# Optimization experiments

Hardware: AMD Instinct MI355X
Metric: run time of the kernel (lower is better)

Reference implementation:

```python
import jax, jax.numpy as jnp
import numpy as np
from jax import lax

B, N, C, CN, M, H, W = 2, 8192, 64, 64, 16, 180, 240
LN_EPS = 1e-5  # torch nn.LayerNorm([C]) default eps


def setup_inputs():
    key = jax.random.key(0)
    ks = jax.random.split(key, 20)
    x = jax.random.uniform(ks[0], (B, N)) * (W - 1)
    y = jax.random.uniform(ks[1], (B, N)) * (H - 1)
    t = jax.random.uniform(ks[2], (B, N))
    p = jnp.where(jax.random.uniform(ks[3], (B, N)) < 0.5, -1.0, 1.0)
    events = jnp.stack([x, y, t, p], axis=-1)  # [B,N,4]
    s = 0.05
    w = lambda k, shape: jax.random.normal(k, shape) * s
    return {
        "events": events,
        "W_mlp1": w(ks[4], (4, C)),
        "W_pe": w(ks[5], (4, CN)),
        "ln_w": jnp.ones((C,)),
        "ln_b": jnp.zeros((C,)),
        "lx_Wq": w(ks[6], (C, CN)), "lx_Wk": w(ks[7], (C, CN)),
        "lx_Wv": w(ks[8], (C, CN)), "lx_Wsa1": w(ks[9], (CN, 1)),
        "lx_Wsa2": w(ks[10], (CN, C)),
        "gx_Wq": w(ks[11], (C, CN)), "gx_Wk": w(ks[12], (C, CN)),
        "gx_Wv": w(ks[13], (C, CN)), "gx_Wpe": w(ks[14], (C, CN)),
        "gx_Wsa1": w(ks[15], (CN, 1)), "gx_Wsa2": w(ks[16], (CN, C)),
    }


def select_nearest(vect, m):
    # torch: F.pad(left=m//2, right=m//2-1) then unfold(dim=1, size=m, step=1)
    b, n, c = vect.shape
    pad = m // 2
    vp = jnp.pad(vect, ((0, 0), (pad, pad - 1), (0, 0)))
    idx = jnp.arange(n)[:, None] + jnp.arange(m)[None, :]  # [N,M]
    return vp[:, idx, :]  # [B,N,M,C]


def fps(event, npoint):
    # faithful farthest_point_sample_batch; masked_select returns the sampled
    # points in ORIGINAL index order, hence the sort of selected indices.
    b, n, c = event.shape
    bary = jnp.mean(event, axis=1, keepdims=True)
    farthest0 = jnp.argmax(jnp.sum((event - bary) ** 2, -1), axis=1)  # [B]
    dist0 = jnp.full((b, n), 1e10, event.dtype)

    def step(carry, _):
        distance, farthest = carry
        centroid = jnp.take_along_axis(event, farthest[:, None, None], axis=1)
        d = jnp.sum((event - centroid) ** 2, -1)
        distance = jnp.minimum(distance, d)  # distance[dist<distance]=dist
        return (distance, jnp.argmax(distance, axis=1)), farthest

    _, sel = lax.scan(step, (dist0, farthest0), None, length=npoint)
    sel = jnp.sort(sel.T, axis=1)  # [B,npoint], sorted index order
    return jnp.take_along_axis(event, sel[:, :, None], axis=1)  # [B,npoint,C]


def sub_attention(q, k_multi, v_multi, pe, Wsa1, Wsa2):
    # sa = q - k + pe -> Linear(Cn,1) -> softmax over M.
    # The original then computes matmul(scores[B,1,N,M], (v+pe)^T[B,Cn,M,N])
    # and sums over the last axis, which is exactly
    #   scores @ (sum_n (v_multi + pe))  -- computed here without the
    # [B,Cn,N,N] intermediate.
    sa = q[:, :, None, :] - k_multi + pe          # [B,N,M,Cn]
    logits = jnp.squeeze(sa @ Wsa1, -1)           # [B,N,M]
    scores = jax.nn.softmax(logits, axis=-1)
    S = jnp.sum(v_multi + pe, axis=1)             # [B,M,Cn]
    p_attn = jnp.einsum("bnm,bmc->bnc", scores, S)
    return p_attn @ Wsa2                          # [B,N,C]


def layer_norm(x, w, b):
    mu = jnp.mean(x, axis=-1, keepdims=True)
    var = jnp.var(x, axis=-1, keepdims=True)
    return (x - mu) / jnp.sqrt(var + LN_EPS) * w + b


def normalize_nonzero(space):
    # mean/std over nonzero entries (std unbiased, ddof=1 as torch.std)
    mask = space != 0
    cnt = jnp.sum(mask)
    mean = jnp.sum(jnp.where(mask, space, 0.0)) / jnp.maximum(cnt, 1)
    var = jnp.sum(jnp.where(mask, (space - mean) ** 2, 0.0)) / jnp.maximum(cnt - 1, 1)
    std = jnp.sqrt(var)
    centered = jnp.where(mask, space - mean, space)
    safe_std = jnp.where(std > 0, std, 1.0)
    normed = jnp.where(std > 0, centered / safe_std, centered)
    return jnp.where(cnt > 0, normed, space)


def events_to_image(feat, ev, ln_w, ln_b):
    # feat [N,C], ev [N,4]
    h = jax.nn.gelu(layer_norm(feat, ln_w, ln_b), approximate=False)
    xi = jnp.floor(ev[:, 0]).astype(jnp.int32)
    yi = jnp.floor(ev[:, 1]).astype(jnp.int32)
    p = ev[:, 3]
    flat = yi * W + xi
    space = jnp.zeros((H * W, h.shape[1]), h.dtype).at[flat].add(p[:, None] * h)
    return normalize_nonzero(space.reshape(H, W, -1))


def reference(events, W_mlp1, W_pe, ln_w, ln_b,
              lx_Wq, lx_Wk, lx_Wv, lx_Wsa1, lx_Wsa2,
              gx_Wq, gx_Wk, gx_Wv, gx_Wpe, gx_Wsa1, gx_Wsa2):
    b, n, _ = events.shape
    lx_in = events @ W_mlp1                                    # [B,N,C]
    # EventTransformer position encoding: unfold-neighbor differences in raw
    # 4-d event space, then Linear(4,Cn)
    pe = (events[:, :, None, :] - select_nearest(events, M)) @ W_pe  # [B,N,M,Cn]
    # LXformer
    q = lx_in @ lx_Wq
    k = lx_in @ lx_Wk
    v = lx_in @ lx_Wv
    lx_sa = sub_attention(q, select_nearest(k, M), select_nearest(v, M),
                          pe, lx_Wsa1, lx_Wsa2)
    lx_out = lx_in + lx_sa
    # GXformer: FPS-sampled global keys/values, FPS-based position encoding
    pe_g = (lx_out[:, :, None, :] - fps(lx_out, M)[:, None, :, :]) @ gx_Wpe
    qg = lx_out @ gx_Wq
    kg = lx_out @ gx_Wk
    vg = lx_out @ gx_Wv
    k_m = jnp.broadcast_to(fps(kg, M)[:, None], (b, n, M, CN))
    v_m = jnp.broadcast_to(fps(vg, M)[:, None], (b, n, M, CN))
    gx_sa = sub_attention(qg, k_m, v_m, pe_g, gx_Wsa1, gx_Wsa2)
    gx_out = lx_out + gx_sa
    # scatter events to image per batch element
    imgs = jax.vmap(lambda f, e: events_to_image(f, e, ln_w, ln_b))(gx_out, events)
    return jnp.transpose(imgs, (0, 3, 1, 2))  # [B,C,H,W]
```

## Files before the change

kernel.cpp:

```cpp
#include <hip/hip_runtime.h>


typedef unsigned short u16;
typedef unsigned long long ull;

#define NB 8192
#define IMG_H 180
#define IMG_W 240
#define HWPIX (IMG_H*IMG_W)
#define SPB (HWPIX*64)
#define NC (NB*64)

#define TT_AC    0
#define TT_T     16384
#define TT_W1    32768
#define TT_EDGEV 32960
#define TT_EDGEF 35008
#define TT_S     37056
#define TT_SEL   39104
#define TT_CG    45248
#define TT_ESUM  45376
#define TT_STATS 45408
#define TT_SYNC  45440
#define TT_GCNT  45632
#define TT_LXS   45664
#define TT_ZOFF  45376
#define TT_ZCNT  288
#define TT_TOT   45792

__device__ __forceinline__ float bf2f(u16 u){
  union { unsigned int i; float f; } w; w.i = ((unsigned int)u) << 16; return w.f;
}
__device__ __forceinline__ u16 f2bf(float f){
  union { unsigned int i; float f; } w; w.f = f;
  unsigned int x = w.i;
  x += 0x7fffu + ((x >> 16) & 1u);
  return (u16)(x >> 16);
}
__device__ __forceinline__ bool isbf(const void* ev){
  unsigned w3 = ((const unsigned*)ev)[3];
  return !(w3 == 0x3F800000u || w3 == 0xBF800000u);
}
__device__ __forceinline__ float ld(const void* p, int i, bool bf){
  return bf ? bf2f(((const u16*)p)[i]) : ((const float*)p)[i];
}
__device__ __forceinline__ void stout(void* o, long i, float v, bool bf){
  if (bf) ((u16*)o)[i] = f2bf(v); else ((float*)o)[i] = v;
}
__device__ __forceinline__ float waveSum(float v){
#pragma unroll
  for (int m = 1; m < 64; m <<= 1) v += __shfl_xor(v, m, 64);
  return v;
}
__device__ __forceinline__ ull waveMaxU64(ull v){
#pragma unroll
  for (int m = 1; m < 64; m <<= 1){
    ull o = (ull)__shfl_xor((long long)v, m, 64);
    if (o > v) v = o;
  }
  return v;
}
__device__ __forceinline__ ull packPDI(int phase, float d, int n){
  return ((ull)phase << 45) | ((ull)__float_as_uint(d) << 13) | (ull)(8191 - n);
}
__device__ __forceinline__ int unpackI(ull p){ return 8191 - (int)(p & 0x1FFFull); }

__global__ void kW(const void* __restrict__ ev, const void* __restrict__ Wq,
                   const void* __restrict__ Wk, const void* __restrict__ Wpe,
                   const void* __restrict__ w1, float* __restrict__ ws, int tail){
  const bool bf = isbf(ev);
  const int tid = threadIdx.x;
  for (int i = tid; i < TT_ZCNT; i += 256) ws[tail + TT_ZOFF + i] = 0.f;
  if (tid < 64){
    float s1 = 0.f, s2 = 0.f;
    for (int c = 0; c < 64; c++){
      float wc = ld(w1, c, bf);
      s1 += ld(Wq, tid*64 + c, bf) * wc;
      s2 += ld(Wk, tid*64 + c, bf) * wc;
    }
    ws[tail + TT_W1 + tid] = s1;
    ws[tail + TT_W1 + 64 + tid] = s2;
    if (tid < 4){
      float s3 = 0.f;
      for (int c = 0; c < 64; c++) s3 += ld(Wpe, tid*64 + c, bf) * ld(w1, c, bf);
      ws[tail + TT_W1 + 128 + tid] = s3;
    }
  }
}

__global__ void __launch_bounds__(256) kE(const void* __restrict__ ev,
    float* __restrict__ ws, int tail, int bb0){
  const bool bf = isbf(ev);
  const int bb = bb0 + blockIdx.z;
  const int lane = threadIdx.x & 63, w = threadIdx.x >> 6;
  float s0 = 0.f, s1 = 0.f, s2 = 0.f, s3 = 0.f;
#pragma unroll
  for (int j = 0; j < 4; j++){
    int r = blockIdx.x*256 + threadIdx.x + 2048*j;
    const int e4 = (bb*NB + r)*4;
    s0 += ld(ev, e4+0, bf); s1 += ld(ev, e4+1, bf);
    s2 += ld(ev, e4+2, bf); s3 += ld(ev, e4+3, bf);
  }
  s0 = waveSum(s0); s1 = waveSum(s1); s2 = waveSum(s2); s3 = waveSum(s3);
  __shared__ float r4[4][4];
  if (lane == 0){ r4[w][0]=s0; r4[w][1]=s1; r4[w][2]=s2; r4[w][3]=s3; }
  __syncthreads();
  if (threadIdx.x < 4)
    atomicAdd(&ws[tail + TT_ESUM + bb*16 + threadIdx.x],
              r4[0][threadIdx.x]+r4[1][threadIdx.x]+r4[2][threadIdx.x]+r4[3][threadIdx.x]);
}

__global__ void __launch_bounds__(256, 4) kA(const void* __restrict__ ev,
    const void* __restrict__ Wm, const void* __restrict__ Wpe,
    const void* __restrict__ Wv, float* __restrict__ ws,
    int offA, int strA, int tail, int bb0){
  const bool bf = isbf(ev);
  const int bb = bb0 + blockIdx.z;
  const int lane = threadIdx.x & 63, w = threadIdx.x >> 6;
  float* A = ws + offA + (size_t)bb*strA;
  const float wq1 = ws[tail + TT_W1 + lane];
  const float wk1 = ws[tail + TT_W1 + 64 + lane];
  const float wp10 = ws[tail+TT_W1+128], wp11 = ws[tail+TT_W1+129],
              wp12 = ws[tail+TT_W1+130], wp13 = ws[tail+TT_W1+131];
  const float wm0 = ld(Wm, 0*64+lane, bf), wm1 = ld(Wm, 1*64+lane, bf),
              wm2 = ld(Wm, 2*64+lane, bf), wm3 = ld(Wm, 3*64+lane, bf);
  const bool edgeBlk = (blockIdx.x == 0 || blockIdx.x == 1023);
#pragma unroll
  for (int i = 0; i < 2; i++){
    const int n = blockIdx.x*8 + w + 4*i;
    const int e4 = (bb*NB + n)*4;
    float e0 = ld(ev, e4+0, bf), e1 = ld(ev, e4+1, bf),
          e2 = ld(ev, e4+2, bf), e3 = ld(ev, e4+3, bf);
    float lx = e0*wm0 + e1*wm1 + e2*wm2 + e3*wm3;
    float epe = e0*wp10 + e1*wp11 + e2*wp12 + e3*wp13;
    float acv = waveSum(lx * wq1) + epe;
    float tv  = waveSum(lx * wk1) + epe;
    A[n*64 + lane] = lx;
    if (lane == 0){
      ws[tail + TT_AC + bb*8192 + n] = acv;
      ws[tail + TT_T  + bb*8192 + n] = tv;
    }
    if (edgeBlk && (n < 8 || n >= NB-8)){
      int e = (n < 8) ? n : (n - (NB-16));
      float v = 0.f;
      for (int cn = 0; cn < 64; cn++)
        v += __shfl(lx, cn, 64) * ld(Wv, cn*64 + lane, bf);
      float f = e0*ld(Wpe, lane, bf) + e1*ld(Wpe, 64+lane, bf)
              + e2*ld(Wpe, 128+lane, bf) + e3*ld(Wpe, 192+lane, bf);
      ws[tail + TT_EDGEV + bb*1024 + e*64 + lane] = v;
      ws[tail + TT_EDGEF + bb*1024 + e*64 + lane] = f;
    }
  }
}

__global__ void __launch_bounds__(64) kB(const void* __restrict__ ev,
    const void* __restrict__ Wm, const void* __restrict__ Wv,
    const void* __restrict__ Wsa2, float* __restrict__ ws, int tail, int bb0){
  const bool bf = isbf(ev);
  const int bb = bb0 + blockIdx.z;
  const int m = blockIdx.x, lane = threadIdx.x;
  float tm = 0.f;
#pragma unroll
  for (int i = 0; i < 4; i++) tm += ws[tail + TT_ESUM + bb*16 + i] * ld(Wm, i*64 + lane, bf);
  float vs0 = 0.f, vs1 = 0.f;
#pragma unroll
  for (int j = 0; j < 64; j += 2){
    vs0 += __shfl(tm, j, 64)   * ld(Wv, j*64 + lane, bf);
    vs1 += __shfl(tm, j+1, 64) * ld(Wv, (j+1)*64 + lane, bf);
  }
  float vsum = vs0 + vs1;
  const int d = m - 8;
  float sv = 0.f, sf = 0.f;
  const float* EV = ws + tail + TT_EDGEV + bb*1024;
  const float* EF = ws + tail + TT_EDGEF + bb*1024;
  if (d < 0){
    for (int e = 16 + d; e < 16; e++){ sv += EV[e*64+lane]; sf += EF[e*64+lane]; }
  } else {
    for (int e = 0; e < d; e++){ sv += EV[e*64+lane]; sf += EF[e*64+lane]; }
  }
  float S = vsum - sv + sf;
  float sw0 = 0.f, sw1 = 0.f;
#pragma unroll
  for (int c = 0; c < 64; c += 2){
    sw0 += __shfl(S, c, 64)   * ld(Wsa2, c*64 + lane, bf);
    sw1 += __shfl(S, c+1, 64) * ld(Wsa2, (c+1)*64 + lane, bf);
  }
  ws[tail + TT_S + bb*1024 + m*64 + lane] = sw0 + sw1;
}

__global__ void __launch_bounds__(256) kC(const void* __restrict__ ev,
    const void* __restrict__ gWk, const void* __restrict__ gWv,
    float* __restrict__ ws,
    int offA, int strA, int offB, int strB, int offC, int strC,
    int offLXP, int strLXP, int tail, int bb0){
  const bool bf = isbf(ev);
  const int bb = bb0 + blockIdx.z;
  float* A = ws + offA + (size_t)bb*strA;
  float* Bp = ws + offB + (size_t)bb*strB;
  float* Cp = ws + offC + (size_t)bb*strC;
  __shared__ float SW_lds[1024];
  __shared__ float WK[4096];
  __shared__ float WV[4096];
  __shared__ float lred[4][64];
  const int tid = threadIdx.x, lane = tid & 63, w = tid >> 6;
  for (int i = tid; i < 1024; i += 256) SW_lds[i] = ws[tail + TT_S + bb*1024 + i];
  for (int i = tid; i < 4096; i += 256){
    WK[i] = ld(gWk, i, bf);
    WV[i] = ld(gWv, i, bf);
  }
  __syncthreads();
  float lxoR[2];
  float lxsum = 0.f;
#pragma unroll
  for (int i = 0; i < 2; i++){
    const int n = blockIdx.x*8 + w + 4*i;
    float lx  = A[n*64 + lane];
    float acn = ws[tail + TT_AC + bb*8192 + n];
    const int m = lane & 15;
    const int j = n + m - 8;
    float tv = (j >= 0 && j < NB) ? ws[tail + TT_T + bb*8192 + j] : 0.f;
    float logit = acn - tv;
    float mx = logit;
#pragma unroll
    for (int k = 1; k < 16; k <<= 1) mx = fmaxf(mx, __shfl_xor(mx, k, 64));
    float ex = expf(logit - mx);
    float sm = ex;
#pragma unroll
    for (int k = 1; k < 16; k <<= 1) sm += __shfl_xor(sm, k, 64);
    float sig = ex / sm;
    float sa = 0.f;
#pragma unroll
    for (int mm = 0; mm < 16; mm++) sa += __shfl(sig, mm, 64) * SW_lds[mm*64 + lane];
    float lxo = lx + sa;
    lxoR[i] = lxo;
    Bp[n*64 + lane] = lxo;
    lxsum += lxo;
  }
  lred[w][lane] = lxsum;
#pragma unroll
  for (int i = 0; i < 2; i++){
    const int n = blockIdx.x*8 + w + 4*i;
    float k0 = 0.f, k1 = 0.f, v0 = 0.f, v1 = 0.f;
#pragma unroll
    for (int cn = 0; cn < 64; cn += 2){
      float x0 = __shfl(lxoR[i], cn, 64);
      float x1 = __shfl(lxoR[i], cn+1, 64);
      k0 += x0 * WK[cn*64 + lane];
      k1 += x1 * WK[(cn+1)*64 + lane];
      v0 += x0 * WV[cn*64 + lane];
      v1 += x1 * WV[(cn+1)*64 + lane];
    }
    A[n*64 + lane] = k0 + k1;
    Cp[n*64 + lane] = v0 + v1;
  }
  __syncthreads();
  if (tid < 64)
    ws[offLXP + (size_t)bb*strLXP + blockIdx.x*64 + tid] =
      lred[0][tid]+lred[1][tid]+lred[2][tid]+lred[3][tid];
}

__global__ void __launch_bounds__(512) kL(float* __restrict__ ws,
    int offLXP, int strLXP, int tail, int bb0){
  const int bb = bb0 + blockIdx.z;
  __shared__ float red[8][64];
  const int tid = threadIdx.x, c = tid & 63, grp = tid >> 6;
  const float* LXP = ws + offLXP + (size_t)bb*strLXP;
  float s = 0.f;
  for (int b2 = grp; b2 < 1024; b2 += 8) s += LXP[b2*64 + c];
  red[grp][c] = s;
  __syncthreads();
  if (tid < 64){
    float t = 0.f;
#pragma unroll
    for (int q = 0; q < 8; q++) t += red[q][tid];
    ws[tail + TT_LXS + bb*64 + tid] = t;
  }
}

__global__ void __launch_bounds__(512) kFPS(const void* __restrict__ ev,
    const void* __restrict__ gWk, const void* __restrict__ gWv,
    const void* __restrict__ gWpe, const void* __restrict__ gWsa1,
    const void* __restrict__ gWsa2, float* __restrict__ ws,
    int offA, int strA, int offB, int strB, int offC, int strC,
    int tail, int bb0){
  const int g = blockIdx.y, idx = blockIdx.x;
  const int bb = bb0 + blockIdx.z;
  const int tid = threadIdx.x, lane = tid & 63, w = tid >> 6;
  const float* pts = ws + (g == 0 ? offB + (size_t)bb*strB
                         : g == 1 ? offA + (size_t)bb*strA
                                  : offC + (size_t)bb*strC);
  ull* slot = (ull*)(ws + tail + TT_SYNC + (bb*3 + g)*32);
  int* gcnt = (int*)(ws + tail + TT_GCNT + bb*16);

  __shared__ float cent[64];
  __shared__ float lxsS[64];
  __shared__ ull   wvS[8];
  __shared__ int   selS[16];
  __shared__ int   sCur;
  __shared__ float gfS[1024];
  __shared__ float betaS[16];
  __shared__ float GS[64];

  const int n0 = idx*1024 + tid;
  float4 P[2][16];
#pragma unroll
  for (int j = 0; j < 2; j++)
#pragma unroll
    for (int i = 0; i < 16; i++)
      P[j][i] = ((const float4*)(pts + (size_t)(n0 + j*512)*64))[i];

  const bool bf = isbf(ev);
  if (tid < 64){
    float lxs = ws[tail + TT_LXS + bb*64 + tid];
    lxsS[tid] = lxs;
    float c;
    if (g == 0) c = lxs * (1.0f/NB);
    else {
      const void* W = (g == 1) ? gWk : gWv;
      float s = 0.f;
#pragma unroll
      for (int j = 0; j < 64; j++) s += __shfl(lxs, j, 64) * ld(W, j*64 + tid, bf);
      c = s * (1.0f/NB);
    }
    cent[tid] = c;
  }
  __syncthreads();

  const float4* cv = (const float4*)cent;
  float md[2] = {1e10f, 1e10f};
  int cur;

  {
    float dd[2];
#pragma unroll
    for (int j = 0; j < 2; j++){
      float d = 0.f;
#pragma unroll
      for (int i = 0; i < 16; i++){
        float4 c = cv[i];
        float dx = P[j][i].x-c.x, dy = P[j][i].y-c.y, dz = P[j][i].z-c.z, dw = P[j][i].w-c.w;
        d += dx*dx; d += dy*dy; d += dz*dz; d += dw*dw;
      }
      dd[j] = d;
    }
    ull p0 = packPDI(1, dd[0], n0);
    ull p1 = packPDI(1, dd[1], n0 + 512);
    ull bp = waveMaxU64(p0 > p1 ? p0 : p1);
    if (lane == 0) wvS[w] = bp;
    __syncthreads();
    if (w == 0){
      ull v = (lane < 8) ? wvS[lane] : 0;
#pragma unroll
      for (int m = 1; m < 8; m <<= 1){
        ull o = (ull)__shfl_xor((long long)v, m, 64);
        if (o > v) v = o;
      }
      if (lane == 0)
        __hip_atomic_store(&slot[8 + idx], v, __ATOMIC_RELEASE, __HIP_MEMORY_SCOPE_AGENT);
      ull got;
      for (;;){
        got = (lane < 8) ? __hip_atomic_load(&slot[8 + lane], __ATOMIC_RELAXED, __HIP_MEMORY_SCOPE_AGENT) : 0;
        ull ok = __ballot(lane >= 8 || (int)(got >> 45) == 1);
        if (ok == ~0ull) break;
        __builtin_amdgcn_s_sleep(1);
      }
#pragma unroll
      for (int m = 1; m < 8; m <<= 1){
        ull o = (ull)__shfl_xor((long long)got, m, 64);
        if (o > got) got = o;
      }
      if (lane == 0) sCur = unpackI(got);
    }
    __syncthreads();
    cur = sCur;
  }

  for (int it = 0; ; it++){
    if (tid == 0) selS[it] = cur;
    if (it == 15) break;
    if (tid < 16) ((float4*)cent)[tid] = ((const float4*)(pts + (size_t)cur*64))[tid];
    __syncthreads();
    const int phase = it + 2;
    float dd[2];
#pragma unroll
    for (int j = 0; j < 2; j++){
      float d = 0.f;
#pragma unroll
      for (int i = 0; i < 16; i++){
        float4 c = cv[i];
        float dx = P[j][i].x-c.x, dy = P[j][i].y-c.y, dz = P[j][i].z-c.z, dw = P[j][i].w-c.w;
        d += dx*dx; d += dy*dy; d += dz*dz; d += dw*dw;
      }
      md[j] = fminf(md[j], d);
      dd[j] = md[j];
    }
    ull p0 = packPDI(phase, dd[0], n0);
    ull p1 = packPDI(phase, dd[1], n0 + 512);
    ull bp = waveMaxU64(p0 > p1 ? p0 : p1);
    if (lane == 0) wvS[w] = bp;
    __syncthreads();
    const int par = phase & 1;
    if (w == 0){
      ull v = (lane < 8) ? wvS[lane] : 0;
#pragma unroll
      for (int m = 1; m < 8; m <<= 1){
        ull o = (ull)__shfl_xor((long long)v, m, 64);
        if (o > v) v = o;
      }
      if (lane == 0)
        __hip_atomic_store(&slot[par*8 + idx], v, __ATOMIC_RELEASE, __HIP_MEMORY_SCOPE_AGENT);
      ull got;
      for (;;){
        got = (lane < 8) ? __hip_atomic_load(&slot[par*8 + lane], __ATOMIC_RELAXED, __HIP_MEMORY_SCOPE_AGENT) : 0;
        ull ok = __ballot(lane >= 8 || (int)(got >> 45) == phase);
        if (ok == ~0ull) break;
        __builtin_amdgcn_s_sleep(1);
      }
#pragma unroll
      for (int m = 1; m < 8; m <<= 1){
        ull o = (ull)__shfl_xor((long long)got, m, 64);
        if (o > got) got = o;
      }
      if (lane == 0) sCur = unpackI(got);
    }
    __syncthreads();
    cur = sCur;
  }
  __syncthreads();

  if (idx == 0){
    if (tid == 0){
      for (int i = 1; i < 16; i++){
        int key = selS[i]; int j = i - 1;
        while (j >= 0 && selS[j] > key){ selS[j+1] = selS[j]; j--; }
        selS[j+1] = key;
      }
    }
    __syncthreads();
    for (int idx2 = tid; idx2 < 1024; idx2 += 512)
      ws[tail + TT_SEL + bb*3072 + g*1024 + idx2] = pts[(size_t)selS[idx2 >> 6]*64 + (idx2 & 63)];
    __threadfence();
  }
  __syncthreads();
  if (tid == 0) atomicAdd(gcnt, 1);
  if (g != 0 || idx != 0) return;

  if (tid == 0){
    while (__hip_atomic_load(gcnt, __ATOMIC_RELAXED, __HIP_MEMORY_SCOPE_AGENT) < 24)
      __builtin_amdgcn_s_sleep(1);
    __threadfence();
  }
  __syncthreads();
  if (tid < 64){
    const float gw1 = ld(gWsa1, tid, bf);
    float wpec[64];
#pragma unroll
    for (int cn = 0; cn < 64; cn++) wpec[cn] = ld(gWpe, cn*64 + tid, bf);
    float lxs = lxsS[tid];
    float G = 0.f;
#pragma unroll
    for (int cn = 0; cn < 64; cn++) G += __shfl(lxs, cn, 64) * wpec[cn];
    GS[tid] = G;
    const float* selp = ws + tail + TT_SEL + bb*3072;
    for (int m = 0; m < 16; m++){
      float plx = selp[m*64 + tid];
      float g2 = 0.f;
#pragma unroll
      for (int cn = 0; cn < 64; cn++) g2 += __shfl(plx, cn, 64) * wpec[cn];
      gfS[m*64 + tid] = g2;
      float pkv = selp[1024 + m*64 + tid];
      float part = waveSum((pkv + g2) * gw1);
      if (tid == 0) betaS[m] = part;
    }
  }
  __syncthreads();
  if (tid < 64){
    float mx = -1e30f;
    for (int m = 0; m < 16; m++) mx = fmaxf(mx, -betaS[m]);
    float ssum = 0.f;
    for (int m = 0; m < 16; m++) ssum += expf(-betaS[m] - mx);
    float A = 0.f;
    for (int m = 0; m < 16; m++){
      float sg = expf(-betaS[m] - mx) / ssum;
      float pv = ws[tail + TT_SEL + bb*3072 + 2048 + m*64 + tid];
      float Sg = 8192.0f * (pv - gfS[m*64 + tid]) + GS[tid];
      A += sg * Sg;
    }
    float cg = 0.f;
#pragma unroll
    for (int cn = 0; cn < 64; cn++) cg += __shfl(A, cn, 64) * ld(gWsa2, cn*64 + tid, bf);
    ws[tail + TT_CG + bb*64 + tid] = cg;
  }
}

__global__ void kZeroSpace(float* __restrict__ ws, int offSp, int strSp, int bb0){
  const int bb = bb0 + blockIdx.z;
  float4 z = make_float4(0.f, 0.f, 0.f, 0.f);
  ((float4*)(ws + offSp + (size_t)bb*strSp))[blockIdx.x*256 + threadIdx.x] = z;
}

__global__ void __launch_bounds__(256, 4) kImg(const void* __restrict__ ev,
    const void* __restrict__ lnw, const void* __restrict__ lnb,
    float* __restrict__ ws, int offB, int strB, int offSp, int strSp,
    int tail, int bb0){
  const bool bf = isbf(ev);
  const int bb = bb0 + blockIdx.z;
  const int lane = threadIdx.x & 63, w = threadIdx.x >> 6;
  const float cg = ws[tail + TT_CG + bb*64 + lane];
  const float lw = ld(lnw, lane, bf), lb = ld(lnb, lane, bf);
  float* space = ws + offSp + (size_t)bb*strSp;
  const float* Bp = ws + offB + (size_t)bb*strB;
#pragma unroll
  for (int i = 0; i < 2; i++){
    const int n = blockIdx.x*8 + w + 4*i;
    float x = Bp[n*64 + lane] + cg;
    float mu = waveSum(x) * (1.0f/64.0f);
    float dv = x - mu;
    float var = waveSum(dv*dv) * (1.0f/64.0f);
    float xn = dv / sqrtf(var + 1e-5f);
    float y = xn * lw + lb;
    float h = 0.5f * y * (1.0f + erff(y * 0.70710678118654752f));
    const int e4 = (bb*NB + n)*4;
    float exf = ld(ev, e4+0, bf), eyf = ld(ev, e4+1, bf), epf = ld(ev, e4+3, bf);
    int xi = (int)floorf(exf), yi = (int)floorf(eyf);
    int flat = yi*IMG_W + xi;
    flat = max(0, min(HWPIX-1, flat));
    atomicAdd(space + flat*64 + lane, epf * h);
  }
}

__global__ void __launch_bounds__(256) kStat(float* __restrict__ ws,
    int offSp, int strSp, int tail, int bb0){
  const int bb = bb0 + blockIdx.z;
  const float4* sp = (const float4*)(ws + offSp + (size_t)bb*strSp);
  float cnt = 0.f, sum = 0.f, ssq = 0.f;
  for (unsigned i = blockIdx.x*256u + threadIdx.x; i < SPB/4; i += 65536u){
    float4 v = sp[i];
    if (v.x != 0.f){ cnt += 1.f; sum += v.x; ssq += v.x*v.x; }
    if (v.y != 0.f){ cnt += 1.f; sum += v.y; ssq += v.y*v.y; }
    if (v.z != 0.f){ cnt += 1.f; sum += v.z; ssq += v.z*v.z; }
    if (v.w != 0.f){ cnt += 1.f; sum += v.w; ssq += v.w*v.w; }
  }
  cnt = waveSum(cnt); sum = waveSum(sum); ssq = waveSum(ssq);
  __shared__ float rc[4], rs[4], rq[4];
  const int lane = threadIdx.x & 63, w = threadIdx.x >> 6;
  if (lane == 0){ rc[w] = cnt; rs[w] = sum; rq[w] = ssq; }
  __syncthreads();
  if (threadIdx.x == 0){
    atomicAdd(&ws[tail + TT_STATS + bb*16 + 0], rc[0]+rc[1]+rc[2]+rc[3]);
    atomicAdd(&ws[tail + TT_STATS + bb*16 + 1], rs[0]+rs[1]+rs[2]+rs[3]);
    atomicAdd(&ws[tail + TT_STATS + bb*16 + 2], rq[0]+rq[1]+rq[2]+rq[3]);
  }
}

__global__ void __launch_bounds__(256) kOut(const void* __restrict__ ev,
    const float* __restrict__ ws, void* __restrict__ out,
    int offSp, int strSp, int tail, int bb0){
  const bool bf = isbf(ev);
  const int bb = bb0 + blockIdx.z;
  __shared__ float tile[64*64];
  const int tid = threadIdx.x;
  const int hw0 = blockIdx.x*64;
  const float* sp = ws + offSp + (size_t)bb*strSp;
#pragma unroll
  for (int i = 0; i < 16; i++){
    int idx = tid + 256*i;
    tile[idx] = sp[(size_t)hw0*64 + idx];
  }
  const float cnt = ws[tail + TT_STATS + bb*16 + 0];
  const float sum = ws[tail + TT_STATS + bb*16 + 1];
  const float ssq = ws[tail + TT_STATS + bb*16 + 2];
  const float mean = sum / fmaxf(cnt, 1.f);
  const float m2   = fmaxf(ssq - sum*mean, 0.f);
  const float var  = m2 / fmaxf(cnt - 1.f, 1.f);
  const float stdv = sqrtf(var);
  __syncthreads();
  const int c = tid >> 2, sub = tid & 3;
#pragma unroll
  for (int j = 0; j < 16; j++){
    int hwl = sub*16 + j;
    float x = tile[hwl*64 + c];
    float centered = (x != 0.f) ? (x - mean) : x;
    float normed = (stdv > 0.f) ? (centered / stdv) : centered;
    float o = (cnt > 0.f) ? normed : x;
    stout(out, (long)(bb*64 + c)*HWPIX + hw0 + hwl, o, bf);
  }
}

extern "C" void kernel_launch(void* const* d_in, const int* in_sizes, int n_in,
                              void* d_out, int out_size, void* d_ws, size_t ws_size,
                              hipStream_t stream){
  (void)in_sizes; (void)n_in; (void)out_size;
  const void* ev     = d_in[0];
  const void* Wm     = d_in[1];
  const void* Wpe    = d_in[2];
  const void* lnw    = d_in[3];
  const void* lnb    = d_in[4];
  const void* lxWq   = d_in[5];
  const void* lxWk   = d_in[6];
  const void* lxWv   = d_in[7];
  const void* lxWsa1 = d_in[8];
  const void* lxWsa2 = d_in[9];
  const void* gxWk   = d_in[11];
  const void* gxWv   = d_in[12];
  const void* gxWpe  = d_in[13];
  const void* gxWsa1 = d_in[14];
  const void* gxWsa2 = d_in[15];
  float* ws = (float*)d_ws;

  const int P_TAIL = 2*NC + 2*SPB;
  const size_t PAR_BYTES = (size_t)(P_TAIL + TT_TOT) * 4;
  const bool par = ws_size >= PAR_BYTES;

  int offB, strB, offSp, strSp, offA, strA, offC, strC, offLXP, strLXP, tail;
  if (par){
    offB = 0;        strB = NC;
    offSp = 2*NC;    strSp = SPB;
    offA = 2*NC;     strA = NC;
    offC = 4*NC;     strC = NC;
    offLXP = 6*NC;   strLXP = 65536;
    tail = P_TAIL;
  } else {
    offSp = 0;       strSp = 0;
    offA = 0;        strA = 0;
    offC = NC;       strC = 0;
    offLXP = 2*NC;   strLXP = 0;
    offB = SPB;      strB = 0;
    tail = SPB + NC;
  }
  const int nb = par ? 2 : 1;
  const int iters = par ? 1 : 2;

  kW<<<1, 256, 0, stream>>>(ev, lxWq, lxWk, Wpe, lxWsa1, ws, tail);
  for (int t = 0; t < iters; t++){
    const int bb0 = par ? 0 : t;
    kE<<<dim3(8,1,nb), 256, 0, stream>>>(ev, ws, tail, bb0);
    kA<<<dim3(1024,1,nb), 256, 0, stream>>>(ev, Wm, Wpe, lxWv, ws, offA, strA, tail, bb0);
    kB<<<dim3(16,1,nb), 64, 0, stream>>>(ev, Wm, lxWv, lxWsa2, ws, tail, bb0);
    kC<<<dim3(1024,1,nb), 256, 0, stream>>>(ev, gxWk, gxWv, ws,
        offA, strA, offB, strB, offC, strC, offLXP, strLXP, tail, bb0);
    kL<<<dim3(1,1,nb), 512, 0, stream>>>(ws, offLXP, strLXP, tail, bb0);
    kFPS<<<dim3(8,3,nb), 512, 0, stream>>>(ev, gxWk, gxWv, gxWpe, gxWsa1, gxWsa2, ws,
        offA, strA, offB, strB, offC, strC, tail, bb0);
    kZeroSpace<<<dim3(2700,1,nb), 256, 0, stream>>>(ws, offSp, strSp, bb0);
    kImg<<<dim3(1024,1,nb), 256, 0, stream>>>(ev, lnw, lnb, ws, offB, strB, offSp, strSp, tail, bb0);
    kStat<<<dim3(256,1,nb), 256, 0, stream>>>(ws, offSp, strSp, tail, bb0);
    kOut<<<dim3(675,1,nb), 256, 0, stream>>>(ev, ws, d_out, offSp, strSp, tail, bb0);
  }
}
```

Baseline: 345.4 us.

## Fuse event sum into kA and overlap image zeroing with FPS blocks

```diff
diff --git a/kernel.cpp b/kernel.cpp
--- a/kernel.cpp
+++ b/kernel.cpp
@@ -88,28 +88,6 @@
   }
 }
 
-__global__ void __launch_bounds__(256) kE(const void* __restrict__ ev,
-    float* __restrict__ ws, int tail, int bb0){
-  const bool bf = isbf(ev);
-  const int bb = bb0 + blockIdx.z;
-  const int lane = threadIdx.x & 63, w = threadIdx.x >> 6;
-  float s0 = 0.f, s1 = 0.f, s2 = 0.f, s3 = 0.f;
-#pragma unroll
-  for (int j = 0; j < 4; j++){
-    int r = blockIdx.x*256 + threadIdx.x + 2048*j;
-    const int e4 = (bb*NB + r)*4;
-    s0 += ld(ev, e4+0, bf); s1 += ld(ev, e4+1, bf);
-    s2 += ld(ev, e4+2, bf); s3 += ld(ev, e4+3, bf);
-  }
-  s0 = waveSum(s0); s1 = waveSum(s1); s2 = waveSum(s2); s3 = waveSum(s3);
-  __shared__ float r4[4][4];
-  if (lane == 0){ r4[w][0]=s0; r4[w][1]=s1; r4[w][2]=s2; r4[w][3]=s3; }
-  __syncthreads();
-  if (threadIdx.x < 4)
-    atomicAdd(&ws[tail + TT_ESUM + bb*16 + threadIdx.x],
-              r4[0][threadIdx.x]+r4[1][threadIdx.x]+r4[2][threadIdx.x]+r4[3][threadIdx.x]);
-}
-
 __global__ void __launch_bounds__(256, 4) kA(const void* __restrict__ ev,
     const void* __restrict__ Wm, const void* __restrict__ Wpe,
     const void* __restrict__ Wv, float* __restrict__ ws,
@@ -125,12 +103,14 @@
   const float wm0 = ld(Wm, 0*64+lane, bf), wm1 = ld(Wm, 1*64+lane, bf),
               wm2 = ld(Wm, 2*64+lane, bf), wm3 = ld(Wm, 3*64+lane, bf);
   const bool edgeBlk = (blockIdx.x == 0 || blockIdx.x == 1023);
+  float es0 = 0.f, es1 = 0.f, es2 = 0.f, es3 = 0.f;
 #pragma unroll
   for (int i = 0; i < 2; i++){
     const int n = blockIdx.x*8 + w + 4*i;
     const int e4 = (bb*NB + n)*4;
     float e0 = ld(ev, e4+0, bf), e1 = ld(ev, e4+1, bf),
           e2 = ld(ev, e4+2, bf), e3 = ld(ev, e4+3, bf);
+    es0 += e0; es1 += e1; es2 += e2; es3 += e3;
     float lx = e0*wm0 + e1*wm1 + e2*wm2 + e3*wm3;
     float epe = e0*wp10 + e1*wp11 + e2*wp12 + e3*wp13;
     float acv = waveSum(lx * wq1) + epe;
@@ -151,6 +131,14 @@
       ws[tail + TT_EDGEF + bb*1024 + e*64 + lane] = f;
     }
   }
+  es0 = waveSum(es0) * (1.0f/64.0f); es1 = waveSum(es1) * (1.0f/64.0f);
+  es2 = waveSum(es2) * (1.0f/64.0f); es3 = waveSum(es3) * (1.0f/64.0f);
+  __shared__ float r4[4][4];
+  if (lane == 0){ r4[w][0]=es0; r4[w][1]=es1; r4[w][2]=es2; r4[w][3]=es3; }
+  __syncthreads();
+  if (threadIdx.x < 4)
+    atomicAdd(&ws[tail + TT_ESUM + bb*16 + threadIdx.x],
+              r4[0][threadIdx.x]+r4[1][threadIdx.x]+r4[2][threadIdx.x]+r4[3][threadIdx.x]);
 }
 
 __global__ void __launch_bounds__(64) kB(const void* __restrict__ ev,
@@ -277,12 +265,19 @@
   }
 }
 
-__global__ void __launch_bounds__(512) kFPS(const void* __restrict__ ev,
+__global__ void __launch_bounds__(512, 1) kFPS(const void* __restrict__ ev,
     const void* __restrict__ gWk, const void* __restrict__ gWv,
     const void* __restrict__ gWpe, const void* __restrict__ gWsa1,
     const void* __restrict__ gWsa2, float* __restrict__ ws,
     int offA, int strA, int offB, int strB, int offC, int strC,
-    int tail, int bb0){
+    int offSp, int zeroCnt, int zplane, int tail, int bb0){
+  if (blockIdx.x >= 4){
+    unsigned zid = (blockIdx.x - 4) + (unsigned)zplane*(blockIdx.y + 3u*blockIdx.z);
+    unsigned i = zid*512u + threadIdx.x;
+    if (i < (unsigned)zeroCnt)
+      ((float4*)(ws + offSp))[i] = make_float4(0.f, 0.f, 0.f, 0.f);
+    return;
+  }
   const int g = blockIdx.y, idx = blockIdx.x;
   const int bb = bb0 + blockIdx.z;
   const int tid = threadIdx.x, lane = tid & 63, w = tid >> 6;
@@ -301,13 +296,13 @@
   __shared__ float betaS[16];
   __shared__ float GS[64];
 
-  const int n0 = idx*1024 + tid;
-  float4 P[2][16];
-#pragma unroll
-  for (int j = 0; j < 2; j++)
+  const int n0 = idx*512 + tid;
+  float4 P[4][16];
+#pragma unroll
+  for (int j = 0; j < 4; j++)
 #pragma unroll
     for (int i = 0; i < 16; i++)
-      P[j][i] = ((const float4*)(pts + (size_t)(n0 + j*512)*64))[i];
+      P[j][i] = ((const float4*)(pts + (size_t)(n0 + j*2048)*64))[i];
 
   const bool bf = isbf(ev);
   if (tid < 64){
@@ -327,13 +322,13 @@
   __syncthreads();
 
   const float4* cv = (const float4*)cent;
-  float md[2] = {1e10f, 1e10f};
+  float md[4] = {1e10f, 1e10f, 1e10f, 1e10f};
   int cur;
 
   {
-    float dd[2];
-#pragma unroll
-    for (int j = 0; j < 2; j++){
+    ull mp = 0;
+#pragma unroll
+    for (int j = 0; j < 4; j++){
       float d = 0.f;
 #pragma unroll
       for (int i = 0; i < 16; i++){
@@ -341,11 +336,10 @@
         float dx = P[j][i].x-c.x, dy = P[j][i].y-c.y, dz = P[j][i].z-c.z, dw = P[j][i].w-c.w;
         d += dx*dx; d += dy*dy; d += dz*dz; d += dw*dw;
       }
-      dd[j] = d;
-    }
-    ull p0 = packPDI(1, dd[0], n0);
-    ull p1 = packPDI(1, dd[1], n0 + 512);
-    ull bp = waveMaxU64(p0 > p1 ? p0 : p1);
+      ull p = packPDI(1, d, n0 + j*2048);
+      if (p > mp) mp = p;
+    }
+    ull bp = waveMaxU64(mp);
     if (lane == 0) wvS[w] = bp;
     __syncthreads();
     if (w == 0){
@@ -356,16 +350,16 @@
         if (o > v) v = o;
       }
       if (lane == 0)
-        __hip_atomic_store(&slot[8 + idx], v, __ATOMIC_RELEASE, __HIP_MEMORY_SCOPE_AGENT);
+        __hip_atomic_store(&slot[4 + idx], v, __ATOMIC_RELEASE, __HIP_MEMORY_SCOPE_AGENT);
       ull got;
       for (;;){
-        got = (lane < 8) ? __hip_atomic_load(&slot[8 + lane], __ATOMIC_RELAXED, __HIP_MEMORY_SCOPE_AGENT) : 0;
-        ull ok = __ballot(lane >= 8 || (int)(got >> 45) == 1);
+        got = (lane < 4) ? __hip_atomic_load(&slot[4 + lane], __ATOMIC_RELAXED, __HIP_MEMORY_SCOPE_AGENT) : 0;
+        ull ok = __ballot(lane >= 4 || (int)(got >> 45) == 1);
         if (ok == ~0ull) break;
         __builtin_amdgcn_s_sleep(1);
       }
 #pragma unroll
-      for (int m = 1; m < 8; m <<= 1){
+      for (int m = 1; m < 4; m <<= 1){
         ull o = (ull)__shfl_xor((long long)got, m, 64);
         if (o > got) got = o;
       }
@@ -381,9 +375,9 @@
     if (tid < 16) ((float4*)cent)[tid] = ((const float4*)(pts + (size_t)cur*64))[tid];
     __syncthreads();
     const int phase = it + 2;
-    float dd[2];
-#pragma unroll
-    for (int j = 0; j < 2; j++){
+    ull mp = 0;
+#pragma unroll
+    for (int j = 0; j < 4; j++){
       float d = 0.f;
 #pragma unroll
       for (int i = 0; i < 16; i++){
@@ -392,11 +386,10 @@
         d += dx*dx; d += dy*dy; d += dz*dz; d += dw*dw;
       }
       md[j] = fminf(md[j], d);
-      dd[j] = md[j];
-    }
-    ull p0 = packPDI(phase, dd[0], n0);
-    ull p1 = packPDI(phase, dd[1], n0 + 512);
-    ull bp = waveMaxU64(p0 > p1 ? p0 : p1);
+      ull p = packPDI(phase, md[j], n0 + j*2048);
+      if (p > mp) mp = p;
+    }
+    ull bp = waveMaxU64(mp);
     if (lane == 0) wvS[w] = bp;
     __syncthreads();
     const int par = phase & 1;
@@ -408,16 +401,16 @@
         if (o > v) v = o;
       }
       if (lane == 0)
-        __hip_atomic_store(&slot[par*8 + idx], v, __ATOMIC_RELEASE, __HIP_MEMORY_SCOPE_AGENT);
+        __hip_atomic_store(&slot[par*4 + idx], v, __ATOMIC_RELEASE, __HIP_MEMORY_SCOPE_AGENT);
       ull got;
       for (;;){
-        got = (lane < 8) ? __hip_atomic_load(&slot[par*8 + lane], __ATOMIC_RELAXED, __HIP_MEMORY_SCOPE_AGENT) : 0;
-        ull ok = __ballot(lane >= 8 || (int)(got >> 45) == phase);
+        got = (lane < 4) ? __hip_atomic_load(&slot[par*4 + lane], __ATOMIC_RELAXED, __HIP_MEMORY_SCOPE_AGENT) : 0;
+        ull ok = __ballot(lane >= 4 || (int)(got >> 45) == phase);
         if (ok == ~0ull) break;
         __builtin_amdgcn_s_sleep(1);
       }
 #pragma unroll
-      for (int m = 1; m < 8; m <<= 1){
+      for (int m = 1; m < 4; m <<= 1){
         ull o = (ull)__shfl_xor((long long)got, m, 64);
         if (o > got) got = o;
       }
@@ -446,7 +439,7 @@
   if (g != 0 || idx != 0) return;
 
   if (tid == 0){
-    while (__hip_atomic_load(gcnt, __ATOMIC_RELAXED, __HIP_MEMORY_SCOPE_AGENT) < 24)
+    while (__hip_atomic_load(gcnt, __ATOMIC_RELAXED, __HIP_MEMORY_SCOPE_AGENT) < 12)
       __builtin_amdgcn_s_sleep(1);
     __threadfence();
   }
@@ -608,12 +601,25 @@
   const void* gxWsa2 = d_in[15];
   float* ws = (float*)d_ws;
 
+  const int F_LXP  = 6*NC;
+  const int F_SP   = 6*NC + 131072;
+  const int F_TAIL = F_SP + 2*SPB;
+  const size_t FULL_BYTES = (size_t)(F_TAIL + TT_TOT) * 4;
   const int P_TAIL = 2*NC + 2*SPB;
   const size_t PAR_BYTES = (size_t)(P_TAIL + TT_TOT) * 4;
-  const bool par = ws_size >= PAR_BYTES;
+
+  const bool full = ws_size >= FULL_BYTES;
+  const bool par  = full || ws_size >= PAR_BYTES;
 
   int offB, strB, offSp, strSp, offA, strA, offC, strC, offLXP, strLXP, tail;
-  if (par){
+  if (full){
+    offB = 0;        strB = NC;
+    offA = 2*NC;     strA = NC;
+    offC = 4*NC;     strC = NC;
+    offLXP = F_LXP;  strLXP = 65536;
+    offSp = F_SP;    strSp = SPB;
+    tail = F_TAIL;
+  } else if (par){
     offB = 0;        strB = NC;
     offSp = 2*NC;    strSp = SPB;
     offA = 2*NC;     strA = NC;
@@ -630,19 +636,22 @@
   }
   const int nb = par ? 2 : 1;
   const int iters = par ? 1 : 2;
+  const int zeroCnt = full ? (2*SPB/4) : 0;
+  const int zplane  = 450;
+  const int zx      = full ? 450 : 0;
 
   kW<<<1, 256, 0, stream>>>(ev, lxWq, lxWk, Wpe, lxWsa1, ws, tail);
   for (int t = 0; t < iters; t++){
     const int bb0 = par ? 0 : t;
-    kE<<<dim3(8,1,nb), 256, 0, stream>>>(ev, ws, tail, bb0);
     kA<<<dim3(1024,1,nb), 256, 0, stream>>>(ev, Wm, Wpe, lxWv, ws, offA, strA, tail, bb0);
     kB<<<dim3(16,1,nb), 64, 0, stream>>>(ev, Wm, lxWv, lxWsa2, ws, tail, bb0);
     kC<<<dim3(1024,1,nb), 256, 0, stream>>>(ev, gxWk, gxWv, ws,
         offA, strA, offB, strB, offC, strC, offLXP, strLXP, tail, bb0);
     kL<<<dim3(1,1,nb), 512, 0, stream>>>(ws, offLXP, strLXP, tail, bb0);
-    kFPS<<<dim3(8,3,nb), 512, 0, stream>>>(ev, gxWk, gxWv, gxWpe, gxWsa1, gxWsa2, ws,
-        offA, strA, offB, strB, offC, strC, tail, bb0);
-    kZeroSpace<<<dim3(2700,1,nb), 256, 0, stream>>>(ws, offSp, strSp, bb0);
+    kFPS<<<dim3(4+zx, 3, nb), 512, 0, stream>>>(ev, gxWk, gxWv, gxWpe, gxWsa1, gxWsa2, ws,
+        offA, strA, offB, strB, offC, strC, offSp, zeroCnt, zplane, tail, bb0);
+    if (!full)
+      kZeroSpace<<<dim3(2700,1,nb), 256, 0, stream>>>(ws, offSp, strSp, bb0);
     kImg<<<dim3(1024,1,nb), 256, 0, stream>>>(ev, lnw, lnb, ws, offB, strB, offSp, strSp, tail, bb0);
     kStat<<<dim3(256,1,nb), 256, 0, stream>>>(ws, offSp, strSp, tail, bb0);
     kOut<<<dim3(675,1,nb), 256, 0, stream>>>(ev, ws, d_out, offSp, strSp, tail, bb0);
```

Result: slower. 465.3 us (+34.7%).
